# Kernel optimization log

Hardware: AMD Instinct MI355X
Metric: run time of the kernel (lower is better)

## Reference

```python
import jax, jax.numpy as jnp
import numpy as np
import math

DIM = 192
D_CONV = 3
EXPAND = 2
D_INNER = EXPAND * DIM          # 384
D_STATE = 1                     # hard-coded in MambaLayer: StructureAwareSSM(..., d_state=1, ...)
DT_RANK = math.ceil(DIM / 16)   # 12
B_, H_, W_ = 16, 96, 96
EPS = 1e-5


def setup_inputs() -> dict:
    key = jax.random.key(0)
    ks = jax.random.split(key, 12)
    s = 0.02
    return {
        "x": jax.random.normal(ks[0], (B_, H_, W_, DIM), jnp.float32),
        "ln_w": jnp.ones((DIM,), jnp.float32),
        "ln_b": jnp.zeros((DIM,), jnp.float32),
        "W_in": jax.random.normal(ks[1], (DIM, 2 * D_INNER), jnp.float32) * s,
        "conv_w": jax.random.normal(ks[2], (D_INNER, 1, D_CONV), jnp.float32) * s,
        "conv_b": jnp.zeros((D_INNER,), jnp.float32),
        "W_xproj": jax.random.normal(ks[3], (D_INNER, DT_RANK + 2 * D_STATE), jnp.float32) * s,
        "W_dt": jax.random.normal(ks[4], (DT_RANK, D_INNER), jnp.float32) * s,
        "b_dt": jax.random.normal(ks[5], (D_INNER,), jnp.float32) * s,
        "A_log": jnp.log(jax.random.uniform(ks[6], (D_INNER, D_STATE), jnp.float32, 0.5, 1.5)),
        "D": jnp.ones((D_INNER,), jnp.float32),
        "W_out": jax.random.normal(ks[7], (D_INNER, DIM), jnp.float32) * s,
    }


def _layernorm(x, w, b):
    mu = x.mean(-1, keepdims=True)
    var = jnp.mean(jnp.square(x - mu), axis=-1, keepdims=True)
    return (x - mu) * jax.lax.rsqrt(var + EPS) * w + b


def _mamba(xs, W_in, conv_w, conv_b, W_xproj, W_dt, b_dt, A_log, D, W_out):
    # xs: (B, L, C)
    b, L, c = xs.shape
    xz = xs @ W_in                                  # (B,L,2*di)
    xb, z = jnp.split(xz, 2, axis=-1)
    # causal depthwise conv over sequence dim
    xc = jax.lax.conv_general_dilated(
        xb.transpose(0, 2, 1),                      # (B,di,L)
        conv_w,                                     # (di,1,k)
        window_strides=(1,),
        padding=[(D_CONV - 1, 0)],
        dimension_numbers=("NCH", "OIH", "NCH"),
        feature_group_count=D_INNER,
    ) + conv_b[None, :, None]
    u = jax.nn.silu(xc).transpose(0, 2, 1)          # (B,L,di)
    proj = u @ W_xproj                              # (B,L,dt_rank+2*ds)
    dt_r = proj[..., :DT_RANK]
    B_ssm = proj[..., DT_RANK:DT_RANK + D_STATE]    # (B,L,ds)
    C_ssm = proj[..., DT_RANK + D_STATE:]           # (B,L,ds)
    dt = jax.nn.softplus(dt_r @ W_dt + b_dt)        # (B,L,di)
    A = -jnp.exp(A_log)                             # (di,ds)
    dA = jnp.exp(dt[..., None] * A)                             # (B,L,di,ds)
    dBu = dt[..., None] * B_ssm[:, :, None, :] * u[..., None]   # (B,L,di,ds)

    def step(h, inp):
        dA_t, dBu_t = inp
        h = dA_t * h + dBu_t
        return h, h

    h0 = jnp.zeros((b, D_INNER, D_STATE), xs.dtype)
    _, hs = jax.lax.scan(step, h0, (dA.transpose(1, 0, 2, 3), dBu.transpose(1, 0, 2, 3)))
    # hs: (L,B,di,ds); contract over state with C
    y = jnp.einsum("lbis,bls->bli", hs, C_ssm)      # (B,L,di)
    y = y + u * D
    y = y * jax.nn.silu(z)
    return y @ W_out                                # (B,L,C)


def reference(x, ln_w, ln_b, W_in, conv_w, conv_b, W_xproj, W_dt, b_dt, A_log, D, W_out):
    b, h, w, c = x.shape
    xn = _layernorm(x, ln_w, ln_b)
    xs = xn.reshape(b, h * w, c)
    y = _mamba(xs, W_in, conv_w, conv_b, W_xproj, W_dt, b_dt, A_log, D, W_out)
    return y.reshape(b, h, w, c) + x
```

## Files before the change

kernel.cpp:

```cpp
#include <hip/hip_runtime.h>
#include <math.h>

#define DIMC 192
#define DIN 384
#define XZC 768
#define NPROJ 14
#define PSTR 16
#define LSEQ 9216
#define NBATCH 16
#define NTOK (NBATCH*LSEQ)
#define CHUNK 128
#define NCH (LSEQ/CHUNK)

typedef unsigned short u16;
typedef unsigned int u32;
typedef __attribute__((ext_vector_type(8))) short bf16x8;
typedef __attribute__((ext_vector_type(4))) float f32x4;

#define AS1 __attribute__((address_space(1)))
#define AS3 __attribute__((address_space(3)))

__device__ __forceinline__ float bf2f(u16 a){
  union { u32 u; float f; } v; v.u = ((u32)a)<<16; return v.f;
}
__device__ __forceinline__ u16 f2bf(float f){
  union { u32 u; float f; } v; v.f = f;
  u32 r = v.u + 0x7FFFu + ((v.u>>16)&1u);
  return (u16)(r>>16);
}
__device__ __forceinline__ float frcp(float x){ return __builtin_amdgcn_rcpf(x); }
__device__ __forceinline__ float softplus_f(float x){
  return fmaxf(x, 0.f) + __logf(1.f + __expf(-fabsf(x)));
}
__device__ __forceinline__ float silu_f(float a){
  return a * frcp(1.f + __expf(-a));
}

__global__ void k_convert(const float* __restrict__ Win, const float* __restrict__ Wout,
                          const float* __restrict__ Wx, const float* __restrict__ cw,
                          u16* __restrict__ Bp1, u16* __restrict__ Bp2,
                          u16* __restrict__ Wxp, float* __restrict__ cwT){
  int i = blockIdx.x*256 + threadIdx.x;
  if (i < XZC*DIMC){
    int j = i&7, lane = (i>>3)&63, rest = i>>9;
    int ks = rest%6, nt = rest/6;
    int k = ks*32 + (lane>>4)*8 + j, n = nt*16 + (lane&15);
    Bp1[i] = f2bf(Win[(size_t)k*XZC + n]);
  }
  if (i < DIN*DIMC){
    int j = i&7, lane = (i>>3)&63, rest = i>>9;
    int ks = rest%12, nt = rest/12;
    int k = ks*32 + (lane>>4)*8 + j, n = nt*16 + (lane&15);
    Bp2[i] = f2bf(Wout[(size_t)k*DIMC + n]);
  }
  if (i < 12*4*16*8){
    int j = i&7, n = (i>>3)&15, quad = (i>>7)&3, kstep = i>>9;
    int k = kstep*32 + quad*8 + j;
    Wxp[i] = (n < NPROJ) ? f2bf(Wx[k*NPROJ + n]) : (u16)0;
  }
  if (i < 3*DIN){
    int tap = i / DIN, ch = i - tap*DIN;
    cwT[i] = cw[ch*3 + tap];
  }
}

__global__ __launch_bounds__(512, 4) void k_lngemm1(const float* __restrict__ x,
        const float* __restrict__ lnw, const float* __restrict__ lnb,
        const u16* __restrict__ Bp1, u16* __restrict__ xB, u16* __restrict__ zB)
{
  __shared__ __align__(16) char smem[49152];
  int tid = threadIdx.x, wv = tid>>6, lane = tid&63;
  int lr = lane&15, lq = lane>>4;
  int tokw = blockIdx.x*256 + wv*32;
  {
    const char* gsrc = (const char*)Bp1 + tid*16;
    char* ldst = smem + wv*1024 + lane*16;
    #pragma unroll
    for (int r=0;r<6;++r)
      __builtin_amdgcn_global_load_lds((const AS1 void*)(gsrc + r*8192),
                                       (AS3 void*)(ldst + r*8192), 16, 0, 0);
  }
  bf16x8 af[2][6];
  #pragma unroll
  for (int s=0;s<2;++s){
    int token = tokw + s*16 + lr;
    const float* xp = x + (size_t)token*DIMC + lq*8;
    float v[48];
    #pragma unroll
    for (int ks=0;ks<6;++ks){
      float4 a = *(const float4*)(xp + ks*32);
      float4 b = *(const float4*)(xp + ks*32 + 4);
      v[ks*8+0]=a.x; v[ks*8+1]=a.y; v[ks*8+2]=a.z; v[ks*8+3]=a.w;
      v[ks*8+4]=b.x; v[ks*8+5]=b.y; v[ks*8+6]=b.z; v[ks*8+7]=b.w;
    }
    float sm = 0.f;
    #pragma unroll
    for (int j=0;j<48;++j) sm += v[j];
    sm += __shfl_xor(sm, 16); sm += __shfl_xor(sm, 32);
    float mu = sm * (1.0f/DIMC);
    float q = 0.f;
    #pragma unroll
    for (int j=0;j<48;++j){ float d = v[j]-mu; q += d*d; }
    q += __shfl_xor(q, 16); q += __shfl_xor(q, 32);
    float rstd = rsqrtf(q*(1.0f/DIMC) + 1e-5f);
    #pragma unroll
    for (int ks=0;ks<6;++ks){
      const float* wp = lnw + lq*8 + ks*32;
      const float* bp = lnb + lq*8 + ks*32;
      float4 w0 = *(const float4*)(wp),   w1 = *(const float4*)(wp+4);
      float4 b0 = *(const float4*)(bp),   b1 = *(const float4*)(bp+4);
      float wj[8] = {w0.x,w0.y,w0.z,w0.w,w1.x,w1.y,w1.z,w1.w};
      float bj[8] = {b0.x,b0.y,b0.z,b0.w,b1.x,b1.y,b1.z,b1.w};
      #pragma unroll
      for (int j=0;j<8;++j)
        af[s][ks][j] = (short)f2bf((v[ks*8+j]-mu)*rstd*wj[j] + bj[j]);
    }
  }
  for (int p=0; p<6; ++p){
    if (p){
      __syncthreads();
      const char* gsrc = (const char*)Bp1 + (size_t)p*49152 + tid*16;
      char* ldst = smem + wv*1024 + lane*16;
      #pragma unroll
      for (int r=0;r<6;++r)
        __builtin_amdgcn_global_load_lds((const AS1 void*)(gsrc + r*8192),
                                         (AS3 void*)(ldst + r*8192), 16, 0, 0);
    }
    asm volatile("s_waitcnt vmcnt(0)" ::: "memory");
    __syncthreads();
    u16* base = (p < 3) ? xB : zB;
    int cbase = (p < 3) ? p*128 : p*128 - DIN;
    #pragma unroll 2
    for (int ntl=0; ntl<8; ++ntl){
      f32x4 acc0 = (f32x4){0.f,0.f,0.f,0.f};
      f32x4 acc1 = (f32x4){0.f,0.f,0.f,0.f};
      #pragma unroll
      for (int ks=0;ks<6;++ks){
        bf16x8 bf_ = *(const bf16x8*)(smem + ((ntl*6+ks)<<10) + lane*16);
        acc0 = __builtin_amdgcn_mfma_f32_16x16x32_bf16(af[0][ks], bf_, acc0, 0,0,0);
        acc1 = __builtin_amdgcn_mfma_f32_16x16x32_bf16(af[1][ks], bf_, acc1, 0,0,0);
      }
      int cc = cbase + ntl*16 + lr;
      #pragma unroll
      for (int r=0;r<4;++r){
        int row0 = tokw + lq*4 + r;
        base[(size_t)row0*DIN + cc]      = f2bf(acc0[r]);
        base[(size_t)(row0+16)*DIN + cc] = f2bf(acc1[r]);
      }
    }
  }
}

__global__ __launch_bounds__(256) void k_conv(const u16* __restrict__ xB,
        const float* __restrict__ cwT, const float* __restrict__ cb,
        const u16* __restrict__ Wxp, float* __restrict__ proj, u16* __restrict__ uB){
  int tid = threadIdx.x, wv = tid>>6, lane = tid&63;
  int lr = lane&15, lq = lane>>4;
  int tok0 = blockIdx.x*64 + wv*16;
  int token = tok0 + lr;
  int l = token % LSEQ;
  float m1 = (l>=1)?1.f:0.f, m2 = (l>=2)?1.f:0.f;
  int tm1 = (l>=1)? token-1 : token;
  int tm2 = (l>=2)? token-2 : token;
  bf16x8 bfrag[12];
  #pragma unroll
  for (int ks=0;ks<12;++ks)
    bfrag[ks] = *(const bf16x8*)(Wxp + (size_t)ks*512 + (size_t)lane*8);
  f32x4 acc = (f32x4){0.f,0.f,0.f,0.f};
  #pragma unroll
  for (int ks=0;ks<12;++ks){
    int ch0 = ks*32 + lq*8;
    bf16x8 x0 = *(const bf16x8*)(xB + (size_t)token*DIN + ch0);
    bf16x8 x1 = *(const bf16x8*)(xB + (size_t)tm1*DIN + ch0);
    bf16x8 x2 = *(const bf16x8*)(xB + (size_t)tm2*DIN + ch0);
    const float* w2 = cwT + 2*DIN + ch0;
    const float* w1 = cwT + 1*DIN + ch0;
    const float* w0 = cwT + 0*DIN + ch0;
    const float* cbp = cb + ch0;
    bf16x8 af;
    #pragma unroll
    for (int j=0;j<8;++j){
      float a = cbp[j] + w2[j]*bf2f((u16)x0[j])
                       + (w1[j]*m1)*bf2f((u16)x1[j])
                       + (w0[j]*m2)*bf2f((u16)x2[j]);
      af[j] = (short)f2bf(silu_f(a));
    }
    *(bf16x8*)(uB + (size_t)token*DIN + ch0) = af;
    acc = __builtin_amdgcn_mfma_f32_16x16x32_bf16(af, bfrag[ks], acc, 0,0,0);
  }
  #pragma unroll
  for (int r=0;r<4;++r){
    int row = lq*4 + r;
    proj[(size_t)(tok0+row)*PSTR + lr] = acc[r];
  }
}

__global__ __launch_bounds__(384) void k_scan1(const float* __restrict__ proj, const u16* __restrict__ uB,
    const float* __restrict__ Wdt, const float* __restrict__ bdt, const float* __restrict__ Alog,
    float* __restrict__ Pg, float* __restrict__ Hg){
  __shared__ __align__(16) float ps[CHUNK*PSTR];
  int b = blockIdx.y, ch = blockIdx.x, d = threadIdx.x;
  int tok0 = b*LSEQ + ch*CHUNK;
  {
    const float4* src = (const float4*)(proj + (size_t)tok0*PSTR);
    float4* dst = (float4*)ps;
    for (int i = d; i < CHUNK*PSTR/4; i += 384) dst[i] = src[i];
  }
  __syncthreads();
  float wdt[12];
  #pragma unroll
  for (int r=0;r<12;++r) wdt[r] = Wdt[r*DIN+d];
  float bd = bdt[d];
  float Av = -__expf(Alog[d]);
  float h = 0.f, P = 1.f;
  #pragma unroll 4
  for (int il=0; il<CHUNK; ++il){
    float uu = bf2f(uB[(size_t)(tok0+il)*DIN + d]);
    const float4* pq = (const float4*)(ps + il*PSTR);
    float4 q0=pq[0], q1=pq[1], q2=pq[2], q3=pq[3];
    float xv = bd + q0.x*wdt[0]+q0.y*wdt[1]+q0.z*wdt[2]+q0.w*wdt[3]
                  + q1.x*wdt[4]+q1.y*wdt[5]+q1.z*wdt[6]+q1.w*wdt[7]
                  + q2.x*wdt[8]+q2.y*wdt[9]+q2.z*wdt[10]+q2.w*wdt[11];
    float dt = softplus_f(xv);
    float dA = __expf(dt*Av);
    h = dA*h + dt*q3.x*uu;
    P *= dA;
  }
  int o = (b*NCH + ch)*DIN + d;
  Pg[o] = P; Hg[o] = h;
}

__global__ void k_scan2(const float* __restrict__ Pg, const float* __restrict__ Hg,
                        float* __restrict__ hin){
  int idx = blockIdx.x*256 + threadIdx.x;
  int b = idx/DIN, d = idx - b*DIN;
  float run = 0.f;
  #pragma unroll 4
  for (int ch=0; ch<NCH; ++ch){
    int o = (b*NCH+ch)*DIN + d;
    hin[o] = run;
    run = Pg[o]*run + Hg[o];
  }
}

__global__ __launch_bounds__(384) void k_scan3(const float* __restrict__ proj, const u16* __restrict__ uB,
    const float* __restrict__ Wdt, const float* __restrict__ bdt,
    const float* __restrict__ Alog, const float* __restrict__ Dp,
    const float* __restrict__ hin, u16* __restrict__ zB){
  __shared__ __align__(16) float ps[CHUNK*PSTR];
  int b = blockIdx.y, ch = blockIdx.x, d = threadIdx.x;
  int tok0 = b*LSEQ + ch*CHUNK;
  {
    const float4* src = (const float4*)(proj + (size_t)tok0*PSTR);
    float4* dst = (float4*)ps;
    for (int i = d; i < CHUNK*PSTR/4; i += 384) dst[i] = src[i];
  }
  __syncthreads();
  float wdt[12];
  #pragma unroll
  for (int r=0;r<12;++r) wdt[r] = Wdt[r*DIN+d];
  float bd = bdt[d];
  float Av = -__expf(Alog[d]);
  float Dv = Dp[d];
  float h = hin[(b*NCH+ch)*DIN + d];
  #pragma unroll 4
  for (int il=0; il<CHUNK; ++il){
    float uu = bf2f(uB[(size_t)(tok0+il)*DIN + d]);
    const float4* pq = (const float4*)(ps + il*PSTR);
    float4 q0=pq[0], q1=pq[1], q2=pq[2], q3=pq[3];
    float xv = bd + q0.x*wdt[0]+q0.y*wdt[1]+q0.z*wdt[2]+q0.w*wdt[3]
                  + q1.x*wdt[4]+q1.y*wdt[5]+q1.z*wdt[6]+q1.w*wdt[7]
                  + q2.x*wdt[8]+q2.y*wdt[9]+q2.z*wdt[10]+q2.w*wdt[11];
    float dt = softplus_f(xv);
    float dA = __expf(dt*Av);
    h = dA*h + dt*q3.x*uu;
    size_t zo = (size_t)(tok0+il)*DIN + d;
    float zz = bf2f(zB[zo]);
    zB[zo] = f2bf((h*q3.y + uu*Dv)*silu_f(zz));
  }
}

__global__ __launch_bounds__(512, 4) void k_gemm2(const u16* __restrict__ A, const u16* __restrict__ Bp2,
        const float* __restrict__ R, float* __restrict__ C)
{
  __shared__ __align__(16) char smem[49152];
  int tid = threadIdx.x, wv = tid>>6, lane = tid&63;
  int lr = lane&15, lq = lane>>4;
  int tokw = blockIdx.x*128 + wv*16;
  int token = tokw + lr;
  {
    const char* gsrc = (const char*)Bp2 + tid*16;
    char* ldst = smem + wv*1024 + lane*16;
    #pragma unroll
    for (int r=0;r<6;++r)
      __builtin_amdgcn_global_load_lds((const AS1 void*)(gsrc + r*8192),
                                       (AS3 void*)(ldst + r*8192), 16, 0, 0);
  }
  bf16x8 af[12];
  #pragma unroll
  for (int ks=0;ks<12;++ks)
    af[ks] = *(const bf16x8*)(A + (size_t)token*DIN + ks*32 + lq*8);
  for (int p=0; p<3; ++p){
    if (p){
      __syncthreads();
      const char* gsrc = (const char*)Bp2 + (size_t)p*49152 + tid*16;
      char* ldst = smem + wv*1024 + lane*16;
      #pragma unroll
      for (int r=0;r<6;++r)
        __builtin_amdgcn_global_load_lds((const AS1 void*)(gsrc + r*8192),
                                         (AS3 void*)(ldst + r*8192), 16, 0, 0);
    }
    asm volatile("s_waitcnt vmcnt(0)" ::: "memory");
    __syncthreads();
    #pragma unroll 2
    for (int ntl=0; ntl<4; ++ntl){
      int nt = p*4 + ntl;
      f32x4 acc = (f32x4){0.f,0.f,0.f,0.f};
      #pragma unroll
      for (int ks=0;ks<12;++ks){
        bf16x8 bf_ = *(const bf16x8*)(smem + ((ntl*12+ks)<<10) + lane*16);
        acc = __builtin_amdgcn_mfma_f32_16x16x32_bf16(af[ks], bf_, acc, 0,0,0);
      }
      int col = nt*16 + lr;
      #pragma unroll
      for (int r=0;r<4;++r){
        int row = tokw + lq*4 + r;
        size_t o = (size_t)row*DIMC + col;
        C[o] = acc[r] + R[o];
      }
    }
  }
}

extern "C" void kernel_launch(void* const* d_in, const int* in_sizes, int n_in,
                              void* d_out, int out_size, void* d_ws, size_t ws_size,
                              hipStream_t stream) {
  const float* x     = (const float*)d_in[0];
  const float* lnw   = (const float*)d_in[1];
  const float* lnb   = (const float*)d_in[2];
  const float* Win   = (const float*)d_in[3];
  const float* convw = (const float*)d_in[4];
  const float* convb = (const float*)d_in[5];
  const float* Wx    = (const float*)d_in[6];
  const float* Wdt   = (const float*)d_in[7];
  const float* bdt   = (const float*)d_in[8];
  const float* Alog  = (const float*)d_in[9];
  const float* Dp    = (const float*)d_in[10];
  const float* Wout  = (const float*)d_in[11];
  float* out = (float*)d_out;

  char* ws = (char*)d_ws;
  size_t off = 0;
  auto alloc = [&](size_t bytes){ size_t r = off; off += (bytes + 255) & ~(size_t)255; return r; };
  u16*   xB    = (u16*)  (ws + alloc((size_t)NTOK*DIN*2));
  u16*   zB    = (u16*)  (ws + alloc((size_t)NTOK*DIN*2));
  u16*   uB    = (u16*)  (ws + alloc((size_t)NTOK*DIN*2));
  float* proj  = (float*)(ws + alloc((size_t)NTOK*PSTR*4));
  u16*   Bp1   = (u16*)  (ws + alloc((size_t)XZC*DIMC*2));
  u16*   Bp2   = (u16*)  (ws + alloc((size_t)DIN*DIMC*2));
  u16*   Wxp   = (u16*)  (ws + alloc((size_t)12*4*16*8*2));
  float* cwT   = (float*)(ws + alloc((size_t)3*DIN*4));
  float* Pg    = (float*)(ws + alloc((size_t)NBATCH*NCH*DIN*4));
  float* Hg    = (float*)(ws + alloc((size_t)NBATCH*NCH*DIN*4));
  float* hin   = (float*)(ws + alloc((size_t)NBATCH*NCH*DIN*4));

  k_convert<<<576, 256, 0, stream>>>(Win, Wout, Wx, convw, Bp1, Bp2, Wxp, cwT);
  k_lngemm1<<<NTOK/256, 512, 0, stream>>>(x, lnw, lnb, Bp1, xB, zB);
  k_conv<<<NTOK/64, 256, 0, stream>>>(xB, cwT, convb, Wxp, proj, uB);
  {
    dim3 g(NCH, NBATCH);
    k_scan1<<<g, 384, 0, stream>>>(proj, uB, Wdt, bdt, Alog, Pg, Hg);
  }
  k_scan2<<<24, 256, 0, stream>>>(Pg, Hg, hin);
  {
    dim3 g(NCH, NBATCH);
    k_scan3<<<g, 384, 0, stream>>>(proj, uB, Wdt, bdt, Alog, Dp, hin, zB);
  }
  k_gemm2<<<NTOK/128, 512, 0, stream>>>(zB, Bp2, x, out);
}
```

Before: 670.9 us.

## Stage GEMM1 output through LDS for vectorized stores, use larger weight phases

The first GEMM kernel now stages each 32x32 bf16 output tile in a per-wave LDS buffer and writes it to global memory as 16-byte vector stores. Previously it issued scattered 2-byte stores per accumulator element. The weight slab loaded into LDS per phase doubles to 96KB, so there are 3 phases instead of 6 and fewer barriers. The cost is far more LDS per block (about 116KB) and a dropped occupancy hint, which likely limits residency to one block per CU.

New measurement: 650.0 us. 1.03x faster.

```diff
diff --git a/kernel.cpp b/kernel.cpp
--- a/kernel.cpp
+++ b/kernel.cpp
@@ -64,21 +64,22 @@
   }
 }
 
-__global__ __launch_bounds__(512, 4) void k_lngemm1(const float* __restrict__ x,
+__global__ __launch_bounds__(512) void k_lngemm1(const float* __restrict__ x,
         const float* __restrict__ lnw, const float* __restrict__ lnb,
         const u16* __restrict__ Bp1, u16* __restrict__ xB, u16* __restrict__ zB)
 {
-  __shared__ __align__(16) char smem[49152];
+  __shared__ __align__(16) char smem[98304];
+  __shared__ __align__(16) u16 cst[8][32][40];
   int tid = threadIdx.x, wv = tid>>6, lane = tid&63;
   int lr = lane&15, lq = lane>>4;
   int tokw = blockIdx.x*256 + wv*32;
   {
-    const char* gsrc = (const char*)Bp1 + tid*16;
-    char* ldst = smem + wv*1024 + lane*16;
-    #pragma unroll
-    for (int r=0;r<6;++r)
-      __builtin_amdgcn_global_load_lds((const AS1 void*)(gsrc + r*8192),
-                                       (AS3 void*)(ldst + r*8192), 16, 0, 0);
+    const char* gsrc = (const char*)Bp1 + wv*12288 + lane*16;
+    char* ldst = smem + wv*12288;
+    #pragma unroll
+    for (int r=0;r<12;++r)
+      __builtin_amdgcn_global_load_lds((const AS1 void*)(gsrc + r*1024),
+                                       (AS3 void*)(ldst + r*1024), 16, 0, 0);
   }
   bf16x8 af[2][6];
   #pragma unroll
@@ -116,37 +117,47 @@
         af[s][ks][j] = (short)f2bf((v[ks*8+j]-mu)*rstd*wj[j] + bj[j]);
     }
   }
-  for (int p=0; p<6; ++p){
+  for (int p=0; p<3; ++p){
     if (p){
       __syncthreads();
-      const char* gsrc = (const char*)Bp1 + (size_t)p*49152 + tid*16;
-      char* ldst = smem + wv*1024 + lane*16;
-      #pragma unroll
-      for (int r=0;r<6;++r)
-        __builtin_amdgcn_global_load_lds((const AS1 void*)(gsrc + r*8192),
-                                         (AS3 void*)(ldst + r*8192), 16, 0, 0);
+      const char* gsrc = (const char*)Bp1 + (size_t)p*98304 + wv*12288 + lane*16;
+      char* ldst = smem + wv*12288;
+      #pragma unroll
+      for (int r=0;r<12;++r)
+        __builtin_amdgcn_global_load_lds((const AS1 void*)(gsrc + r*1024),
+                                         (AS3 void*)(ldst + r*1024), 16, 0, 0);
     }
     asm volatile("s_waitcnt vmcnt(0)" ::: "memory");
     __syncthreads();
-    u16* base = (p < 3) ? xB : zB;
-    int cbase = (p < 3) ? p*128 : p*128 - DIN;
     #pragma unroll 2
-    for (int ntl=0; ntl<8; ++ntl){
-      f32x4 acc0 = (f32x4){0.f,0.f,0.f,0.f};
-      f32x4 acc1 = (f32x4){0.f,0.f,0.f,0.f};
-      #pragma unroll
-      for (int ks=0;ks<6;++ks){
-        bf16x8 bf_ = *(const bf16x8*)(smem + ((ntl*6+ks)<<10) + lane*16);
-        acc0 = __builtin_amdgcn_mfma_f32_16x16x32_bf16(af[0][ks], bf_, acc0, 0,0,0);
-        acc1 = __builtin_amdgcn_mfma_f32_16x16x32_bf16(af[1][ks], bf_, acc1, 0,0,0);
+    for (int ntp=0; ntp<8; ++ntp){
+      #pragma unroll
+      for (int nt2=0; nt2<2; ++nt2){
+        int ntl = ntp*2 + nt2;
+        f32x4 acc0 = (f32x4){0.f,0.f,0.f,0.f};
+        f32x4 acc1 = (f32x4){0.f,0.f,0.f,0.f};
+        #pragma unroll
+        for (int ks=0;ks<6;++ks){
+          bf16x8 bf_ = *(const bf16x8*)(smem + ((ntl*6+ks)<<10) + lane*16);
+          acc0 = __builtin_amdgcn_mfma_f32_16x16x32_bf16(af[0][ks], bf_, acc0, 0,0,0);
+          acc1 = __builtin_amdgcn_mfma_f32_16x16x32_bf16(af[1][ks], bf_, acc1, 0,0,0);
+        }
+        #pragma unroll
+        for (int r=0;r<4;++r){
+          cst[wv][lq*4+r][nt2*16+lr]      = f2bf(acc0[r]);
+          cst[wv][16+lq*4+r][nt2*16+lr]   = f2bf(acc1[r]);
+        }
       }
-      int cc = cbase + ntl*16 + lr;
-      #pragma unroll
-      for (int r=0;r<4;++r){
-        int row0 = tokw + lq*4 + r;
-        base[(size_t)row0*DIN + cc]      = f2bf(acc0[r]);
-        base[(size_t)(row0+16)*DIN + cc] = f2bf(acc1[r]);
-      }
+      int g = p*8 + ntp;
+      u16* base; int cc;
+      if (g < 12){ base = xB; cc = g*32; } else { base = zB; cc = g*32 - DIN; }
+      int row = lane>>1, h = lane&1;
+      const u16* sp = &cst[wv][row][h*16];
+      u16* gp = base + (size_t)(tokw+row)*DIN + cc + h*16;
+      bf16x8 v0 = *(const bf16x8*)(sp);
+      bf16x8 v1 = *(const bf16x8*)(sp + 8);
+      *(bf16x8*)(gp)     = v0;
+      *(bf16x8*)(gp + 8) = v1;
     }
   }
 }
```
